# Optimization experiments

Hardware: AMD Instinct MI355X
Metric: run time of the kernel (lower is better)

Reference implementation:

```python
import jax, jax.numpy as jnp
import numpy as np

STEP = 0.5     # config.saxs_loss.step (Angstrom bin width of P(r) grid)
DMAX = 100.0   # config.saxs_loss.dmax (max pairwise distance considered)
NBINS = int(DMAX / STEP) + 1  # 201 r-bins
N_RES = 256
N_ATOM = 37


def _compute_saxs(all_atom_pos, all_atom_mask):
    """Differentiable pair-distance distribution P(r) on grid r_k = k*STEP.

    Pairwise distances between all masked atoms are soft-binned (linear
    interpolation between the two neighboring bins, which keeps gradients
    w.r.t. coordinates) and the histogram is normalized to sum to 1.
    """
    x = all_atom_pos.reshape(-1, 3)          # [N, 3], N = N_res*37
    m = all_atom_mask.reshape(-1)            # [N]
    n = x.shape[0]
    # Pairwise distances via Gram trick (avoids [N,N,3] intermediate).
    sq = jnp.sum(x * x, axis=-1)             # [N]
    d2 = sq[:, None] + sq[None, :] - 2.0 * (x @ x.T)   # [N, N]
    d = jnp.sqrt(jnp.maximum(d2, 1e-12))
    # Pair weights: both atoms present, exclude self-pairs.
    w = m[:, None] * m[None, :]
    w = w * (1.0 - jnp.eye(n, dtype=w.dtype))
    # Soft linear binning onto the r-grid (differentiable through frac).
    t = jnp.clip(d / STEP, 0.0, NBINS - 1.000001)
    lo = jnp.floor(t).astype(jnp.int32)
    frac = t - lo.astype(d.dtype)
    hist = jnp.zeros((NBINS,), dtype=d.dtype)
    hist = hist.at[lo.ravel()].add((w * (1.0 - frac)).ravel())
    hist = hist.at[jnp.minimum(lo + 1, NBINS - 1).ravel()].add((w * frac).ravel())
    return hist / (jnp.sum(hist) + 1e-12)


def setup_inputs() -> dict:
    key = jax.random.key(0)
    k1, k2, k3 = jax.random.split(key, 3)
    # True structure: coordinates spread over ~tens of Angstroms.
    true_pos = jax.random.normal(k1, (N_RES, N_ATOM, 3), dtype=jnp.float32) * 10.0
    # Predicted structure: true + small perturbation.
    pred_pos = true_pos + jax.random.normal(k2, (N_RES, N_ATOM, 3), dtype=jnp.float32) * 0.5
    mask = jnp.ones((N_RES, N_ATOM), dtype=jnp.float32)
    return {
        "final_atom_positions": pred_pos,
        "all_atom_positions": true_pos,
        "all_atom_mask": mask,
    }


def reference(final_atom_positions, all_atom_positions, all_atom_mask):
    pred_saxs = _compute_saxs(final_atom_positions, all_atom_mask)
    true_saxs = _compute_saxs(all_atom_positions, all_atom_mask)
    # torch.nn.L1Loss(reduction='sum')
    return jnp.sum(jnp.abs(pred_saxs - true_saxs))
```

## Files before the change

### kernel.cpp

```cpp
#include <hip/hip_runtime.h>


#define TILE    256
#define NTILES  37
#define TPAIRS  (NTILES * (NTILES + 1) / 2)
#define NBINS   201
#define NREP    32
#define RSTRIDE 402
#define HSTRIDE 256
#define QSCALE  32768.0f


template<bool DIAG>
__device__ __forceinline__ void accum_tile(
    const float* __restrict__ pos, const float* __restrict__ mask,
    int aBase, int t, int lane,
    float xj, float yj, float zj, float mjq,
    unsigned int* __restrict__ rep)
{
    #pragma unroll
    for (int c = 0; c < 4; ++c) {
        const int ia = aBase + c * 64 + lane;
        const int cx = __float_as_int(2.0f * pos[3 * ia]);
        const int cy = __float_as_int(2.0f * pos[3 * ia + 1]);
        const int cz = __float_as_int(2.0f * pos[3 * ia + 2]);
        const int cm = __float_as_int(mask[ia]);

        #pragma unroll 4
        for (int i = 0; i < 64; ++i) {
            const float sx = __int_as_float(__builtin_amdgcn_readlane(cx, i));
            const float sy = __int_as_float(__builtin_amdgcn_readlane(cy, i));
            const float sz = __int_as_float(__builtin_amdgcn_readlane(cz, i));
            const float sm = __int_as_float(__builtin_amdgcn_readlane(cm, i));

            const float dx = sx - xj;
            const float dy = sy - yj;
            const float dz = sz - zj;
            const float d2 = fmaf(dx, dx, fmaf(dy, dy, dz * dz));
            const float tt = fminf(__builtin_amdgcn_sqrtf(d2), 200.0f);
            const unsigned lo   = (unsigned)tt;
            const float    frac = __builtin_amdgcn_fractf(tt);
            float wp = sm * mjq;
            if (DIAG) wp = (c * 64 + i < t) ? wp : 0.0f;
            const unsigned q   = (unsigned)fmaf(wp, frac, 0.5f);
            const unsigned tot = (unsigned)(wp + 0.5f);
            const unsigned idx = (lo & 1u) * 201u + lo;
            const unsigned long long pack =
                ((unsigned long long)q << 32) | (unsigned long long)(tot - q);
            atomicAdd((unsigned long long*)&rep[idx], pack);
        }
    }
}

__global__ __launch_bounds__(TILE) void saxs_hist_kernel(
    const float* __restrict__ posPred,
    const float* __restrict__ posTrue,
    const float* __restrict__ mask,
    unsigned long long* __restrict__ gh)
{
    const int t    = threadIdx.x;
    const int lane = t & 63;
    const int s    = blockIdx.y;
    const float* __restrict__ pos = s ? posTrue : posPred;
    unsigned long long* __restrict__ ghist = gh + s * HSTRIDE;

    int p = blockIdx.x;
    int a = 0;
    while (p >= NTILES - a) { p -= NTILES - a; ++a; }
    const int b = a + p;

    __shared__ unsigned long long sHist64[NREP * RSTRIDE / 2];
    unsigned int* sHist = (unsigned int*)sHist64;
    for (int k = t; k < NREP * RSTRIDE; k += TILE) sHist[k] = 0u;

    const int jg = b * TILE + t;
    const float xj = 2.0f * pos[3 * jg];
    const float yj = 2.0f * pos[3 * jg + 1];
    const float zj = 2.0f * pos[3 * jg + 2];
    const float mjq = mask[jg] * QSCALE;

    __syncthreads();

    unsigned int* __restrict__ rep = sHist + (t & (NREP - 1)) * RSTRIDE;

    if (a != b) accum_tile<false>(pos, mask, a * TILE, t, lane, xj, yj, zj, mjq, rep);
    else        accum_tile<true >(pos, mask, a * TILE, t, lane, xj, yj, zj, mjq, rep);

    __syncthreads();

    for (int k = t; k < NBINS; k += TILE) {
        unsigned int acc = 0;
        #pragma unroll
        for (int r = 0; r < NREP; ++r) {
            acc += sHist[r * RSTRIDE + k];
            if (k > 0) acc += sHist[r * RSTRIDE + 202 + k - 1];
        }
        atomicAdd(&ghist[k], (unsigned long long)acc);
    }
}

__global__ void saxs_loss_kernel(const unsigned long long* __restrict__ gh,
                                 float* __restrict__ out)
{
    const int lane = threadIdx.x;
    float hp[4], ht[4];
    float sp = 0.0f, st = 0.0f;
    #pragma unroll
    for (int r = 0; r < 4; ++r) {
        const int k = lane + 64 * r;
        float a = 0.0f, c = 0.0f;
        if (k < NBINS) {
            a = (float)gh[k];
            c = (float)gh[HSTRIDE + k];
        }
        hp[r] = a; ht[r] = c;
        sp += a; st += c;
    }
    #pragma unroll
    for (int off = 32; off > 0; off >>= 1) {
        sp += __shfl_xor(sp, off);
        st += __shfl_xor(st, off);
    }
    sp += 1e-12f;
    st += 1e-12f;
    float l = 0.0f;
    #pragma unroll
    for (int r = 0; r < 4; ++r) l += fabsf(hp[r] / sp - ht[r] / st);
    #pragma unroll
    for (int off = 32; off > 0; off >>= 1) l += __shfl_xor(l, off);
    if (lane == 0) out[0] = l;
}

extern "C" void kernel_launch(void* const* d_in, const int* in_sizes, int n_in,
                              void* d_out, int out_size, void* d_ws, size_t ws_size,
                              hipStream_t stream)
{
    const float* pred = (const float*)d_in[0];
    const float* tru  = (const float*)d_in[1];
    const float* msk  = (const float*)d_in[2];
    float* out = (float*)d_out;
    unsigned long long* ws = (unsigned long long*)d_ws;

    hipMemsetAsync(d_ws, 0, 2 * HSTRIDE * sizeof(unsigned long long), stream);

    dim3 grid(TPAIRS, 2);
    saxs_hist_kernel<<<grid, dim3(TILE), 0, stream>>>(pred, tru, msk, ws);
    saxs_loss_kernel<<<dim3(1), dim3(64), 0, stream>>>(ws, out);
}
```

Baseline: 147.8 us.

## Fuse loss into histogram kernel, halve LDS replicas, use integer mask weights

The separate loss kernel is removed. The last block to finish, found through an atomic counter, now reduces the global histogram and writes the loss, which saves one kernel launch. The number of shared-memory histogram replicas drops from 32 to 16, which cuts LDS zeroing and reduction work and may allow more blocks per CU, at the cost of more atomic contention per replica. The per-pair weight is now built from an integer mask ANDed with a bitmask instead of a float multiply and conversion, which assumes the mask is binary.

```diff
diff --git a/kernel.cpp b/kernel.cpp
--- a/kernel.cpp
+++ b/kernel.cpp
@@ -5,7 +5,7 @@
 #define NTILES  37
 #define TPAIRS  (NTILES * (NTILES + 1) / 2)
 #define NBINS   201
-#define NREP    32
+#define NREP    16
 #define RSTRIDE 402
 #define HSTRIDE 256
 #define QSCALE  32768.0f
@@ -15,7 +15,7 @@
 __device__ __forceinline__ void accum_tile(
     const float* __restrict__ pos, const float* __restrict__ mask,
     int aBase, int t, int lane,
-    float xj, float yj, float zj, float mjq,
+    float xj, float yj, float zj, unsigned vj,
     unsigned int* __restrict__ rep)
 {
     #pragma unroll
@@ -24,14 +24,14 @@
         const int cx = __float_as_int(2.0f * pos[3 * ia]);
         const int cy = __float_as_int(2.0f * pos[3 * ia + 1]);
         const int cz = __float_as_int(2.0f * pos[3 * ia + 2]);
-        const int cm = __float_as_int(mask[ia]);
+        const int cmi = (int)(mask[ia] * QSCALE);
 
         #pragma unroll 4
         for (int i = 0; i < 64; ++i) {
             const float sx = __int_as_float(__builtin_amdgcn_readlane(cx, i));
             const float sy = __int_as_float(__builtin_amdgcn_readlane(cy, i));
             const float sz = __int_as_float(__builtin_amdgcn_readlane(cz, i));
-            const float sm = __int_as_float(__builtin_amdgcn_readlane(cm, i));
+            const unsigned smi = (unsigned)__builtin_amdgcn_readlane(cmi, i);
 
             const float dx = sx - xj;
             const float dy = sy - yj;
@@ -40,10 +40,10 @@
             const float tt = fminf(__builtin_amdgcn_sqrtf(d2), 200.0f);
             const unsigned lo   = (unsigned)tt;
             const float    frac = __builtin_amdgcn_fractf(tt);
-            float wp = sm * mjq;
-            if (DIAG) wp = (c * 64 + i < t) ? wp : 0.0f;
-            const unsigned q   = (unsigned)fmaf(wp, frac, 0.5f);
-            const unsigned tot = (unsigned)(wp + 0.5f);
+            unsigned tot = smi & vj;
+            if (DIAG) tot = (c * 64 + i < t) ? tot : 0u;
+            const float    wpf = (float)tot;
+            const unsigned q   = (unsigned)fmaf(wpf, frac, 0.5f);
             const unsigned idx = (lo & 1u) * 201u + lo;
             const unsigned long long pack =
                 ((unsigned long long)q << 32) | (unsigned long long)(tot - q);
@@ -56,7 +56,9 @@
     const float* __restrict__ posPred,
     const float* __restrict__ posTrue,
     const float* __restrict__ mask,
-    unsigned long long* __restrict__ gh)
+    unsigned long long* __restrict__ gh,
+    unsigned int* __restrict__ counter,
+    float* __restrict__ out)
 {
     const int t    = threadIdx.x;
     const int lane = t & 63;
@@ -77,14 +79,14 @@
     const float xj = 2.0f * pos[3 * jg];
     const float yj = 2.0f * pos[3 * jg + 1];
     const float zj = 2.0f * pos[3 * jg + 2];
-    const float mjq = mask[jg] * QSCALE;
+    const unsigned vj = (mask[jg] != 0.0f) ? 0xFFFFFFFFu : 0u;
 
     __syncthreads();
 
     unsigned int* __restrict__ rep = sHist + (t & (NREP - 1)) * RSTRIDE;
 
-    if (a != b) accum_tile<false>(pos, mask, a * TILE, t, lane, xj, yj, zj, mjq, rep);
-    else        accum_tile<true >(pos, mask, a * TILE, t, lane, xj, yj, zj, mjq, rep);
+    if (a != b) accum_tile<false>(pos, mask, a * TILE, t, lane, xj, yj, zj, vj, rep);
+    else        accum_tile<true >(pos, mask, a * TILE, t, lane, xj, yj, zj, vj, rep);
 
     __syncthreads();
 
@@ -97,38 +99,47 @@
         }
         atomicAdd(&ghist[k], (unsigned long long)acc);
     }
-}
 
-__global__ void saxs_loss_kernel(const unsigned long long* __restrict__ gh,
-                                 float* __restrict__ out)
-{
-    const int lane = threadIdx.x;
-    float hp[4], ht[4];
-    float sp = 0.0f, st = 0.0f;
-    #pragma unroll
-    for (int r = 0; r < 4; ++r) {
-        const int k = lane + 64 * r;
-        float a = 0.0f, c = 0.0f;
-        if (k < NBINS) {
-            a = (float)gh[k];
-            c = (float)gh[HSTRIDE + k];
+    __syncthreads();
+    __shared__ int sLast;
+    if (t == 0) {
+        __threadfence();
+        const unsigned prev = __hip_atomic_fetch_add(
+            counter, 1u, __ATOMIC_ACQ_REL, __HIP_MEMORY_SCOPE_AGENT);
+        sLast = (prev == 2u * TPAIRS - 1u);
+    }
+    __syncthreads();
+    if (sLast && t < 64) {
+        const int ln = t;
+        float hp[4], ht[4];
+        float sp = 0.0f, st = 0.0f;
+        #pragma unroll
+        for (int r = 0; r < 4; ++r) {
+            const int k = ln + 64 * r;
+            float av = 0.0f, cv = 0.0f;
+            if (k < NBINS) {
+                av = (float)__hip_atomic_load(&gh[k],           __ATOMIC_RELAXED,
+                                              __HIP_MEMORY_SCOPE_AGENT);
+                cv = (float)__hip_atomic_load(&gh[HSTRIDE + k], __ATOMIC_RELAXED,
+                                              __HIP_MEMORY_SCOPE_AGENT);
+            }
+            hp[r] = av; ht[r] = cv;
+            sp += av; st += cv;
         }
-        hp[r] = a; ht[r] = c;
-        sp += a; st += c;
+        #pragma unroll
+        for (int off = 32; off > 0; off >>= 1) {
+            sp += __shfl_xor(sp, off);
+            st += __shfl_xor(st, off);
+        }
+        sp += 1e-12f;
+        st += 1e-12f;
+        float l = 0.0f;
+        #pragma unroll
+        for (int r = 0; r < 4; ++r) l += fabsf(hp[r] / sp - ht[r] / st);
+        #pragma unroll
+        for (int off = 32; off > 0; off >>= 1) l += __shfl_xor(l, off);
+        if (ln == 0) out[0] = l;
     }
-    #pragma unroll
-    for (int off = 32; off > 0; off >>= 1) {
-        sp += __shfl_xor(sp, off);
-        st += __shfl_xor(st, off);
-    }
-    sp += 1e-12f;
-    st += 1e-12f;
-    float l = 0.0f;
-    #pragma unroll
-    for (int r = 0; r < 4; ++r) l += fabsf(hp[r] / sp - ht[r] / st);
-    #pragma unroll
-    for (int off = 32; off > 0; off >>= 1) l += __shfl_xor(l, off);
-    if (lane == 0) out[0] = l;
 }
 
 extern "C" void kernel_launch(void* const* d_in, const int* in_sizes, int n_in,
@@ -140,10 +151,10 @@
     const float* msk  = (const float*)d_in[2];
     float* out = (float*)d_out;
     unsigned long long* ws = (unsigned long long*)d_ws;
+    unsigned int* counter = (unsigned int*)(ws + 2 * HSTRIDE);
 
-    hipMemsetAsync(d_ws, 0, 2 * HSTRIDE * sizeof(unsigned long long), stream);
+    hipMemsetAsync(d_ws, 0, (2 * HSTRIDE + 1) * sizeof(unsigned long long), stream);
 
     dim3 grid(TPAIRS, 2);
-    saxs_hist_kernel<<<grid, dim3(TILE), 0, stream>>>(pred, tru, msk, ws);
-    saxs_loss_kernel<<<dim3(1), dim3(64), 0, stream>>>(ws, out);
+    saxs_hist_kernel<<<grid, dim3(TILE), 0, stream>>>(pred, tru, msk, ws, counter, out);
 }
```

After: 145.7 us. Within noise of the previous version (-1.4%).
